# Performance work log

Measured on AMD Instinct MI355X. Metric: run time of the kernel, lower is better.

## Reference

```python
import jax, jax.numpy as jnp
import numpy as np

N, C_IN, H, W = 32, 3, 224, 224
C_OUT, K, STRIDE, PAD = 64, 3, 1, 1


def setup_inputs() -> dict:
    key = jax.random.key(0)
    k1, k2 = jax.random.split(key)
    x = jax.random.normal(k1, (N, C_IN, H, W), dtype=jnp.float32)
    weight = jax.random.normal(k2, (C_OUT, C_IN, K, K), dtype=jnp.float32)
    bias = jnp.zeros((C_OUT,), dtype=jnp.float32)
    return {"x": x, "weight": weight, "bias": bias}


def reference(x, weight, bias):
    # Equivalent to the manual im2col + GEMM: a standard 2D convolution
    # (cross-correlation, as the torch code slides the raw kernel).
    out = jax.lax.conv_general_dilated(
        x, weight,
        window_strides=(STRIDE, STRIDE),
        padding=[(PAD, PAD), (PAD, PAD)],
        dimension_numbers=("NCHW", "OIHW", "NCHW"),
    )
    return out + bias[None, :, None, None]
```

## Files before the change

### kernel.cpp

```cpp
#include <hip/hip_runtime.h>


#define N_IMG 32
#define C_IN 3
#define H_ 224
#define W_ 224
#define C_OUT 64
#define NPIX (H_ * W_)
#define COB 16

__global__ __launch_bounds__(256) void conv3x3_kernel(
    const float* __restrict__ x,
    const float* __restrict__ wgt,
    const float* __restrict__ bias,
    float* __restrict__ out)
{
    const int p = blockIdx.x * 256 + threadIdx.x;
    const int n = blockIdx.y;
    const int h = p / W_;
    const int w = p - h * W_;

    float in_v[27];
    const float* xn = x + (size_t)n * C_IN * NPIX;
#pragma unroll
    for (int ci = 0; ci < 3; ++ci) {
#pragma unroll
        for (int dh = 0; dh < 3; ++dh) {
            const int hh = h + dh - 1;
            const bool hok = (unsigned)hh < (unsigned)H_;
#pragma unroll
            for (int dw = 0; dw < 3; ++dw) {
                const int ww = w + dw - 1;
                const bool ok = hok && ((unsigned)ww < (unsigned)W_);
                in_v[(ci * 3 + dh) * 3 + dw] =
                    ok ? xn[ci * NPIX + hh * W_ + ww] : 0.0f;
            }
        }
    }

    float* outp = out + (size_t)n * C_OUT * NPIX + p;
#pragma unroll
    for (int cb = 0; cb < C_OUT / COB; ++cb) {
        float acc[COB];
#pragma unroll
        for (int i = 0; i < COB; ++i) acc[i] = bias[cb * COB + i];
#pragma unroll
        for (int i = 0; i < COB; ++i) {
            const float* wp = wgt + (size_t)(cb * COB + i) * 27;
#pragma unroll
            for (int k = 0; k < 27; ++k) acc[i] += in_v[k] * wp[k];
        }
#pragma unroll
        for (int i = 0; i < COB; ++i)
            outp[(size_t)(cb * COB + i) * NPIX] = acc[i];
    }
}

extern "C" void kernel_launch(void* const* d_in, const int* in_sizes, int n_in,
                              void* d_out, int out_size, void* d_ws, size_t ws_size,
                              hipStream_t stream) {
    const float* x    = (const float*)d_in[0];
    const float* wgt  = (const float*)d_in[1];
    const float* bias = (const float*)d_in[2];
    float* out = (float*)d_out;

    dim3 grid(NPIX / 256, N_IMG);
    dim3 block(256);
    conv3x3_kernel<<<grid, block, 0, stream>>>(x, wgt, bias, out);
}
```

Baseline: 457.7 us.

## Compute four adjacent pixels per thread with float4 I/O and split output channels across grid

```diff
diff --git a/kernel.cpp b/kernel.cpp
--- a/kernel.cpp
+++ b/kernel.cpp
@@ -7,52 +7,64 @@
 #define W_ 224
 #define C_OUT 64
 #define NPIX (H_ * W_)
+#define W4 (W_ / 4)
+#define STRIPS (NPIX / 4)
 #define COB 16
 
-__global__ __launch_bounds__(256) void conv3x3_kernel(
+__global__ __launch_bounds__(256) void conv3x3_v2(
     const float* __restrict__ x,
     const float* __restrict__ wgt,
     const float* __restrict__ bias,
     float* __restrict__ out)
 {
-    const int p = blockIdx.x * 256 + threadIdx.x;
-    const int n = blockIdx.y;
-    const int h = p / W_;
-    const int w = p - h * W_;
+    const int s  = blockIdx.x * 256 + threadIdx.x;
+    const int n  = blockIdx.y;
+    const int cb = blockIdx.z * COB;
+    const int h  = s / W4;
+    const int w4 = (s - h * W4) * 4;
 
-    float in_v[27];
+    float win[C_IN][3][6];
     const float* xn = x + (size_t)n * C_IN * NPIX;
 #pragma unroll
-    for (int ci = 0; ci < 3; ++ci) {
+    for (int ci = 0; ci < C_IN; ++ci) {
 #pragma unroll
-        for (int dh = 0; dh < 3; ++dh) {
-            const int hh = h + dh - 1;
+        for (int r = 0; r < 3; ++r) {
+            const int hh = h + r - 1;
             const bool hok = (unsigned)hh < (unsigned)H_;
+            const float* row = xn + ci * NPIX + hh * W_;
+            if (hok) {
+                const float4 m = *reinterpret_cast<const float4*>(row + w4);
+                win[ci][r][1] = m.x; win[ci][r][2] = m.y;
+                win[ci][r][3] = m.z; win[ci][r][4] = m.w;
+                win[ci][r][0] = (w4 > 0)      ? row[w4 - 1] : 0.0f;
+                win[ci][r][5] = (w4 + 4 < W_) ? row[w4 + 4] : 0.0f;
+            } else {
 #pragma unroll
-            for (int dw = 0; dw < 3; ++dw) {
-                const int ww = w + dw - 1;
-                const bool ok = hok && ((unsigned)ww < (unsigned)W_);
-                in_v[(ci * 3 + dh) * 3 + dw] =
-                    ok ? xn[ci * NPIX + hh * W_ + ww] : 0.0f;
+                for (int c = 0; c < 6; ++c) win[ci][r][c] = 0.0f;
             }
         }
     }
 
-    float* outp = out + (size_t)n * C_OUT * NPIX + p;
+    float* outp = out + ((size_t)n * C_OUT + cb) * NPIX + h * W_ + w4;
 #pragma unroll
-    for (int cb = 0; cb < C_OUT / COB; ++cb) {
-        float acc[COB];
+    for (int i = 0; i < COB; ++i) {
+        const float* wp = wgt + (size_t)(cb + i) * 27;
+        const float b  = bias[cb + i];
+        float a0 = b, a1 = b, a2 = b, a3 = b;
 #pragma unroll
-        for (int i = 0; i < COB; ++i) acc[i] = bias[cb * COB + i];
+        for (int ci = 0; ci < C_IN; ++ci)
 #pragma unroll
-        for (int i = 0; i < COB; ++i) {
-            const float* wp = wgt + (size_t)(cb * COB + i) * 27;
+            for (int r = 0; r < 3; ++r)
 #pragma unroll
-            for (int k = 0; k < 27; ++k) acc[i] += in_v[k] * wp[k];
-        }
-#pragma unroll
-        for (int i = 0; i < COB; ++i)
-            outp[(size_t)(cb * COB + i) * NPIX] = acc[i];
+                for (int dc = 0; dc < 3; ++dc) {
+                    const float wv = wp[(ci * 3 + r) * 3 + dc];
+                    a0 += win[ci][r][0 + dc] * wv;
+                    a1 += win[ci][r][1 + dc] * wv;
+                    a2 += win[ci][r][2 + dc] * wv;
+                    a3 += win[ci][r][3 + dc] * wv;
+                }
+        float4 o; o.x = a0; o.y = a1; o.z = a2; o.w = a3;
+        *reinterpret_cast<float4*>(outp + (size_t)i * NPIX) = o;
     }
 }
 
@@ -64,7 +76,7 @@
     const float* bias = (const float*)d_in[2];
     float* out = (float*)d_out;
 
-    dim3 grid(NPIX / 256, N_IMG);
+    dim3 grid(STRIPS / 256, N_IMG, C_OUT / COB);
     dim3 block(256);
-    conv3x3_kernel<<<grid, block, 0, stream>>>(x, wgt, bias, out);
+    conv3x3_v2<<<grid, block, 0, stream>>>(x, wgt, bias, out);
 }
```

New measurement: 467.7 us. +2.2%, slower.
